# Performance work log

Measured on AMD Instinct MI355X. Metric: run time of the kernel, lower is better.

## Reference

```python
import jax, jax.numpy as jnp
import numpy as np

N = 20000
IN_CH = 2048      # 64 * (768/24)
HID = 512
LAT = 128
KW = 24           # conv1d kernel == stride
COUT = 64
NEG_SLOPE = 0.2
BN_EPS = 1e-5


def gatv2(x, src, dst, Wl, bl, Wr, br, att, bias, n_nodes):
    # GATv2Conv (PyG semantics, 1 head): e_ij = att . leaky_relu(Wl x_j + Wr x_i)
    xl = x @ Wl + bl                      # [N, out] source-side features
    xr = x @ Wr + br                      # [N, out] target-side features
    e = jax.nn.leaky_relu(xl[src] + xr[dst], NEG_SLOPE) @ att   # [E]
    m = jax.ops.segment_max(e, dst, num_segments=n_nodes)       # per-target max
    a = jnp.exp(e - m[dst])
    s = jax.ops.segment_sum(a, dst, num_segments=n_nodes)
    alpha = a / (s[dst] + 1e-16)
    out = jax.ops.segment_sum(xl[src] * alpha[:, None], dst, num_segments=n_nodes)
    return out + bias


def setup_inputs() -> dict:
    key = jax.random.key(0)
    ks = jax.random.split(key, 16)
    x = jax.random.normal(ks[0], (N, 24, 32), dtype=jnp.float32)
    edge_index = jax.random.randint(ks[1], (2, 320000), 0, N, dtype=jnp.int32)
    sc = 0.02
    return {
        "x": x,
        "edge_index": edge_index,
        "conv_w": jax.random.normal(ks[2], (COUT, KW), dtype=jnp.float32) * sc,
        "conv_b": jnp.zeros((COUT,), dtype=jnp.float32),
        "W1l": jax.random.normal(ks[3], (IN_CH, HID), dtype=jnp.float32) * sc,
        "b1l": jnp.zeros((HID,), dtype=jnp.float32),
        "W1r": jax.random.normal(ks[4], (IN_CH, HID), dtype=jnp.float32) * sc,
        "b1r": jnp.zeros((HID,), dtype=jnp.float32),
        "att1": jax.random.normal(ks[5], (HID,), dtype=jnp.float32) * sc,
        "bias1": jnp.zeros((HID,), dtype=jnp.float32),
        "gamma": jnp.ones((HID,), dtype=jnp.float32),
        "beta": jnp.zeros((HID,), dtype=jnp.float32),
        "W2l": jax.random.normal(ks[6], (HID, LAT), dtype=jnp.float32) * sc,
        "b2l": jnp.zeros((LAT,), dtype=jnp.float32),
        "W2r": jax.random.normal(ks[7], (HID, LAT), dtype=jnp.float32) * sc,
        "b2r": jnp.zeros((LAT,), dtype=jnp.float32),
        "att2": jax.random.normal(ks[8], (LAT,), dtype=jnp.float32) * sc,
        "bias2": jnp.zeros((LAT,), dtype=jnp.float32),
    }


def reference(x, edge_index, conv_w, conv_b, W1l, b1l, W1r, b1r, att1, bias1,
              gamma, beta, W2l, b2l, W2r, b2r, att2, bias2):
    n = x.shape[0]
    # x.transpose(1,2).flatten(1): [N,24,32] -> [N,32,24] -> [N,768]
    flat = jnp.transpose(x, (0, 2, 1)).reshape(n, -1)
    # Conv1d(1,64,24,stride=24): kernel==stride => reshape into segments of 24
    segs = flat.reshape(n, -1, KW)                       # [N, 32, 24]
    conv = jnp.einsum("ntk,ok->not", segs, conv_w) + conv_b[None, :, None]  # [N,64,32]
    h = conv.reshape(n, -1)                              # [N, 2048] (channel-major like torch .view)

    # add self-loops (PyG GATv2Conv default add_self_loops=True)
    loops = jnp.arange(n, dtype=edge_index.dtype)
    src = jnp.concatenate([edge_index[0], loops])
    dst = jnp.concatenate([edge_index[1], loops])

    h = gatv2(h, src, dst, W1l, b1l, W1r, b1r, att1, bias1, n)
    h = jax.nn.relu(h)
    # BatchNorm1d in training mode: batch stats over nodes, biased variance
    mean = jnp.mean(h, axis=0)
    var = jnp.mean((h - mean) ** 2, axis=0)
    h = gamma * (h - mean) / jnp.sqrt(var + BN_EPS) + beta

    mu = gatv2(h, src, dst, W2l, b2l, W2r, b2r, att2, bias2, n)
    return mu
```

## Files before the change

### kernel.cpp

```cpp
#include <hip/hip_runtime.h>
#include <cstdint>
#include <cstddef>
#include <type_traits>

static constexpr int NN   = 20000;
static constexpr int MPAD = 20096;
static constexpr int ERAW = 320000;
static constexpr int ETOT = ERAW + NN;

typedef __attribute__((ext_vector_type(8))) short bf16x8;
typedef __attribute__((ext_vector_type(8))) unsigned short u16x8;
typedef __attribute__((ext_vector_type(4))) float f32x4;

__device__ __forceinline__ unsigned short f2bf(float f) {
  union { float f; unsigned u; } v; v.f = f;
  unsigned r = v.u + 0x7fffu + ((v.u >> 16) & 1u);
  return (unsigned short)(r >> 16);
}
__device__ __forceinline__ float bf2f(unsigned short u) {
  union { unsigned u; float f; } v; v.u = ((unsigned)u) << 16;
  return v.f;
}

__device__ __forceinline__ void gload_lds16(const void* g, void* l) {
  __builtin_amdgcn_global_load_lds(
      (const __attribute__((address_space(1))) unsigned int*)g,
      (__attribute__((address_space(3))) unsigned int*)l, 16, 0, 0);
}

__global__ __launch_bounds__(256) void cast_x_kernel(
    const float* __restrict__ x, unsigned short* __restrict__ xb,
    int* __restrict__ degp, float* __restrict__ stats, float* __restrict__ beff1) {
  int i8 = blockIdx.x * 256 + threadIdx.x;
  if (i8 < NN) degp[i8] = 0;
  if (i8 < 1024) { stats[i8] = 0.f; beff1[i8] = 0.f; }
  size_t base = (size_t)i8 * 8;
  int row = i8 / 96;
  u16x8 o;
  if (row < NN) {
    float4 a = *(const float4*)&x[base];
    float4 b = *(const float4*)&x[base + 4];
    o[0] = f2bf(a.x); o[1] = f2bf(a.y); o[2] = f2bf(a.z); o[3] = f2bf(a.w);
    o[4] = f2bf(b.x); o[5] = f2bf(b.y); o[6] = f2bf(b.z); o[7] = f2bf(b.w);
  } else {
#pragma unroll
    for (int j = 0; j < 8; j++) o[j] = 0;
  }
  *(u16x8*)&xb[base] = o;
}

__global__ __launch_bounds__(256) void weff_kernel(
    const float* __restrict__ conv_w, const float* __restrict__ conv_b,
    const float* __restrict__ W1l, const float* __restrict__ b1l,
    const float* __restrict__ W1r, const float* __restrict__ b1r,
    unsigned short* __restrict__ wc1, float* __restrict__ beff1) {
  __shared__ float ws[64 * 24];
  int t = blockIdx.x;
  int tid = threadIdx.x;
  for (int i = tid; i < 64 * 24; i += 256) ws[i] = conv_w[i];
  __syncthreads();
  int c = blockIdx.y * 128 + (tid >> 1);
  int half = tid & 1;
  const float* W; const float* bb; int cl;
  if (c < 512) { W = W1l; bb = b1l; cl = c; } else { W = W1r; bb = b1r; cl = c - 512; }
  float acc[24];
#pragma unroll
  for (int k = 0; k < 24; k++) acc[k] = 0.f;
  float bacc = (t == 0 && half == 0) ? bb[cl] : 0.f;
  for (int o = half * 32; o < half * 32 + 32; o += 4) {
    float Wv[4];
#pragma unroll
    for (int j = 0; j < 4; j++) Wv[j] = W[(size_t)((o + j) * 32 + t) * 512 + cl];
#pragma unroll
    for (int j = 0; j < 4; j++) {
      bacc += conv_b[o + j] * Wv[j];
#pragma unroll
      for (int k = 0; k < 24; k++) acc[k] += ws[(o + j) * 24 + k] * Wv[j];
    }
  }
#pragma unroll
  for (int k = 0; k < 24; k++) acc[k] += __shfl_xor(acc[k], 1);
  bacc += __shfl_xor(bacc, 1);
  if (half == 0) {
#pragma unroll
    for (int k = 0; k < 24; k++) wc1[(size_t)c * 768 + k * 32 + t] = f2bf(acc[k]);
    atomicAdd(&beff1[c], bacc);
  }
}

__global__ __launch_bounds__(256) void w2fold_kernel(
    const float* __restrict__ stats, const float* __restrict__ gamma,
    const float* __restrict__ beta,
    const float* __restrict__ W2l, const float* __restrict__ b2l,
    const float* __restrict__ W2r, const float* __restrict__ b2r,
    unsigned short* __restrict__ wc2, float* __restrict__ beff2) {
  int c = blockIdx.x;
  const float* W; const float* bb; int cl;
  if (c < 128) { W = W2l; bb = b2l; cl = c; } else { W = W2r; bb = b2r; cl = c - 128; }
  int tid = threadIdx.x, lane = tid & 63, wid = tid >> 6;
  float part = 0.f;
#pragma unroll
  for (int j = 0; j < 2; j++) {
    int k = tid * 2 + j;
    float mean = stats[k] * (1.f / NN);
    float var = stats[512 + k] * (1.f / NN) - mean * mean;
    float rstd = rsqrtf(var + 1e-5f);
    float sc = gamma[k] * rstd;
    float sh = beta[k] - sc * mean;
    float wv = W[(size_t)k * 128 + cl];
    wc2[(size_t)c * 512 + k] = f2bf(sc * wv);
    part += sh * wv;
  }
#pragma unroll
  for (int d = 32; d; d >>= 1) part += __shfl_xor(part, d);
  __shared__ float wsum[4];
  if (lane == 0) wsum[wid] = part;
  __syncthreads();
  if (tid == 0) beff2[c] = bb[cl] + wsum[0] + wsum[1] + wsum[2] + wsum[3];
}

template <typename OutT>
__global__ __launch_bounds__(256, 5) void gemm_kernel(
    const unsigned short* __restrict__ A, const unsigned short* __restrict__ B,
    const float* __restrict__ bias0, const float* __restrict__ bias1,
    OutT* __restrict__ C0, OutT* __restrict__ C1,
    int M, int K, int NT, int nsplit, int swz) {
  __shared__ __align__(16) unsigned short As[128 * 64];
  __shared__ __align__(16) unsigned short Bs[128 * 64];
  int bid = blockIdx.x;
  if (swz) bid = (bid & 7) * (gridDim.x >> 3) + (bid >> 3);
  int tm = bid / NT, tn = bid % NT;
  int tid = threadIdx.x, wid = tid >> 6, lane = tid & 63;
  int wr = wid >> 1, wc = wid & 1;
  const unsigned short* gA = A + (size_t)(tm * 128) * K;
  const unsigned short* gB = B + (size_t)(tn * 128) * K;
  int srow = wid * 8 + (lane >> 3);
  int scol = ((lane & 7) ^ (lane >> 3)) * 8;

  f32x4 acc[4][4];
  f32x4 zero = {0.f, 0.f, 0.f, 0.f};
#pragma unroll
  for (int i = 0; i < 4; i++)
#pragma unroll
    for (int j = 0; j < 4; j++) acc[i][j] = zero;

  int KT = K >> 6;
  for (int kt = 0; kt < KT; ++kt) {
    if (kt) __syncthreads();
    {
      const unsigned short* a0 = gA + (size_t)srow * K + kt * 64 + scol;
      const unsigned short* b0 = gB + (size_t)srow * K + kt * 64 + scol;
#pragma unroll
      for (int i = 0; i < 4; i++)
        gload_lds16(a0 + (size_t)i * 32 * K, &As[i * 2048 + wid * 512]);
#pragma unroll
      for (int i = 0; i < 4; i++)
        gload_lds16(b0 + (size_t)i * 32 * K, &Bs[i * 2048 + wid * 512]);
    }
    asm volatile("s_waitcnt vmcnt(0)" ::: "memory");
    __syncthreads();
#pragma unroll
    for (int kk = 0; kk < 2; kk++) {
      int ko = kk * 32 + (lane >> 4) * 8;
      int kosw = ko ^ ((lane & 7) << 3);
      bf16x8 af[4], bfr[4];
#pragma unroll
      for (int mi = 0; mi < 4; mi++)
        af[mi] = *(const bf16x8*)&As[(wr * 64 + mi * 16 + (lane & 15)) * 64 + kosw];
#pragma unroll
      for (int ni = 0; ni < 4; ni++)
        bfr[ni] = *(const bf16x8*)&Bs[(wc * 64 + ni * 16 + (lane & 15)) * 64 + kosw];
#pragma unroll
      for (int mi = 0; mi < 4; mi++)
#pragma unroll
        for (int ni = 0; ni < 4; ni++)
          acc[mi][ni] = __builtin_amdgcn_mfma_f32_16x16x32_bf16(
              af[mi], bfr[ni], acc[mi][ni], 0, 0, 0);
    }
  }

  int ncol_tile = tn * 128;
  OutT* Cd; const float* bs; int col0;
  if (ncol_tile < nsplit) { Cd = C0; bs = bias0; col0 = ncol_tile; }
  else { Cd = C1; bs = bias1; col0 = ncol_tile - nsplit; }
#pragma unroll
  for (int mi = 0; mi < 4; mi++) {
    int rbase = tm * 128 + wr * 64 + mi * 16 + (lane >> 4) * 4;
#pragma unroll
    for (int ni = 0; ni < 4; ni++) {
      int c = col0 + wc * 64 + ni * 16 + (lane & 15);
      float bv = bs[c];
#pragma unroll
      for (int j = 0; j < 4; j++) {
        int r = rbase + j;
        if (r < M) {
          float v = acc[mi][ni][j] + bv;
          if constexpr (sizeof(OutT) == 2) Cd[(size_t)r * nsplit + c] = f2bf(v);
          else Cd[(size_t)r * nsplit + c] = v;
        }
      }
    }
  }
}

__global__ void hist_kernel(const int* __restrict__ dst, int* deg, int E) {
  int e = blockIdx.x * 256 + threadIdx.x;
  if (e < E) atomicAdd(&deg[dst[e]], 1);
}
__global__ __launch_bounds__(1024) void scan1_kernel(
    const int* __restrict__ deg, int* __restrict__ off, int* __restrict__ btot, int n) {
  __shared__ int wsum[16];
  int tid = threadIdx.x, lane = tid & 63, w = tid >> 6;
  int i = blockIdx.x * 1024 + tid;
  int v = (i < n) ? deg[i] + 1 : 0;
  int s = v;
#pragma unroll
  for (int d = 1; d < 64; d <<= 1) {
    int t = __shfl_up(s, d);
    if (lane >= d) s += t;
  }
  if (lane == 63) wsum[w] = s;
  __syncthreads();
  if (w == 0 && lane < 16) {
    int t = wsum[lane];
#pragma unroll
    for (int d = 1; d < 16; d <<= 1) {
      int u = __shfl_up(t, d);
      if (lane >= d) t += u;
    }
    wsum[lane] = t;
  }
  __syncthreads();
  int incl = (w ? wsum[w - 1] : 0) + s;
  if (i < n) off[i] = incl - v;
  if (tid == 1023) btot[blockIdx.x] = incl;
}
__global__ void scan2_kernel(const int* __restrict__ btot, int* __restrict__ gbase,
                             int* __restrict__ off, int nb, int n) {
  int lane = threadIdx.x;
  int v = lane < nb ? btot[lane] : 0;
  int s = v;
#pragma unroll
  for (int d = 1; d < 64; d <<= 1) {
    int t = __shfl_up(s, d);
    if (lane >= d) s += t;
  }
  if (lane < nb) gbase[lane] = s - v;
  if (lane == nb - 1) off[n] = s;
}
__global__ __launch_bounds__(1024) void scan3_kernel(
    int* __restrict__ off, int* __restrict__ cursor,
    const int* __restrict__ gbase, int* __restrict__ esrc, int n) {
  int i = blockIdx.x * 1024 + threadIdx.x;
  if (i < n) {
    int v = off[i] + gbase[blockIdx.x];
    off[i] = v;
    cursor[i] = v + 1;
    esrc[v] = i;
  }
}
__global__ void scatter_kernel(const int* __restrict__ src, const int* __restrict__ dst,
                               int* cursor, int* __restrict__ esrc, int E) {
  int e = blockIdx.x * 256 + threadIdx.x;
  if (e < E) {
    int pos = atomicAdd(&cursor[dst[e]], 1);
    esrc[pos] = src[e];
  }
}

template <int VPL, typename OutT>
__global__ __launch_bounds__(256) void gat_agg_kernel(
    const unsigned short* __restrict__ xl, const unsigned short* __restrict__ xr,
    const float* __restrict__ att, const float* __restrict__ bias,
    const int* __restrict__ off, const int* __restrict__ esrc,
    OutT* __restrict__ out, int n, int do_relu) {
  constexpr int C = VPL * 64;
  using RawT = std::conditional_t<VPL == 8, uint4, unsigned int>;
  int node = blockIdx.x * 4 + (threadIdx.x >> 6);
  int lane = threadIdx.x & 63;
  int base = lane * VPL;
  if (node >= n) {
#pragma unroll
    for (int v = 0; v < VPL; v++) out[(size_t)node * C + base + v] = OutT(0);
    return;
  }
  float xrv[VPL], attv[VPL];
#pragma unroll
  for (int v = 0; v < VPL; v++) {
    xrv[v] = bf2f(xr[(size_t)node * C + base + v]);
    attv[v] = att[base + v];
  }
  auto cvt = [](RawT r, float* xv) {
    if constexpr (VPL == 8) {
      unsigned u[4] = {r.x, r.y, r.z, r.w};
#pragma unroll
      for (int i = 0; i < 4; i++) {
        xv[2 * i]     = __uint_as_float(u[i] << 16);
        xv[2 * i + 1] = __uint_as_float(u[i] & 0xffff0000u);
      }
    } else {
      xv[0] = __uint_as_float(r << 16);
      xv[1] = __uint_as_float(r & 0xffff0000u);
    }
  };
  auto score = [&](const float* xv) {
    float p = 0.f;
#pragma unroll
    for (int v = 0; v < VPL; v++) {
      float t = xv[v] + xrv[v];
      p += attv[v] * fmaxf(t, 0.2f * t);
    }
    return p;
  };
  float s0 = 0.f, s1 = 0.f;
  float acc0[VPL], acc1[VPL];
#pragma unroll
  for (int v = 0; v < VPL; v++) { acc0[v] = 0.f; acc1[v] = 0.f; }
  int e0 = off[node], e1 = off[node + 1];
  int e = e0;
  for (; e + 3 < e1; e += 4) {
    int s0i = esrc[e], s1i = esrc[e + 1], s2i = esrc[e + 2], s3i = esrc[e + 3];
    RawT r0 = *(const RawT*)(xl + (size_t)s0i * C + base);
    RawT r1 = *(const RawT*)(xl + (size_t)s1i * C + base);
    RawT r2 = *(const RawT*)(xl + (size_t)s2i * C + base);
    RawT r3 = *(const RawT*)(xl + (size_t)s3i * C + base);
    float x0[VPL], x1[VPL], x2[VPL], x3[VPL];
    cvt(r0, x0); cvt(r1, x1); cvt(r2, x2); cvt(r3, x3);
    float p0 = score(x0), p1 = score(x1), p2 = score(x2), p3 = score(x3);
    p0 += __shfl_xor(p0, 32); p1 += __shfl_xor(p1, 32);
    p2 += __shfl_xor(p2, 32); p3 += __shfl_xor(p3, 32);
    float a = (lane & 32) ? p1 : p0;
    float b = (lane & 32) ? p3 : p2;
    a += __shfl_xor(a, 16); b += __shfl_xor(b, 16);
    float cpk = (lane & 16) ? b : a;
    cpk += __shfl_xor(cpk, 8); cpk += __shfl_xor(cpk, 4);
    cpk += __shfl_xor(cpk, 2); cpk += __shfl_xor(cpk, 1);
    float w = __expf(cpk);
    float w0 = __shfl(w, 0),  w2 = __shfl(w, 16);
    float w1 = __shfl(w, 32), w3 = __shfl(w, 48);
    s0 += w0 + w2; s1 += w1 + w3;
#pragma unroll
    for (int v = 0; v < VPL; v++) {
      acc0[v] += w0 * x0[v] + w2 * x2[v];
      acc1[v] += w1 * x1[v] + w3 * x3[v];
    }
  }
  for (; e < e1; ++e) {
    RawT r0 = *(const RawT*)(xl + (size_t)esrc[e] * C + base);
    float x0[VPL];
    cvt(r0, x0);
    float p0 = score(x0);
#pragma unroll
    for (int d2 = 32; d2; d2 >>= 1) p0 += __shfl_xor(p0, d2);
    float w0 = __expf(p0);
    s0 += w0;
#pragma unroll
    for (int v = 0; v < VPL; v++) acc0[v] += w0 * x0[v];
  }
  float inv = 1.f / (s0 + s1 + 1e-16f);
#pragma unroll
  for (int v = 0; v < VPL; v++) {
    float o = (acc0[v] + acc1[v]) * inv + bias[base + v];
    if (do_relu) o = fmaxf(o, 0.f);
    if constexpr (sizeof(OutT) == 2) out[(size_t)node * C + base + v] = f2bf(o);
    else out[(size_t)node * C + base + v] = o;
  }
}

__global__ __launch_bounds__(256) void bn_stats_kernel(
    const unsigned short* __restrict__ h1, float* __restrict__ stats, int n) {
  int tid = threadIdx.x;
  int c0 = tid * 2;
  int r0 = blockIdx.x * 64;
  int r1 = r0 + 64 < n ? r0 + 64 : n;
  float s0 = 0, q0 = 0, s1 = 0, q1 = 0;
  for (int r = r0; r < r1; ++r) {
    unsigned u = *(const unsigned*)&h1[(size_t)r * 512 + c0];
    float a = __uint_as_float(u << 16);
    float b = __uint_as_float(u & 0xffff0000u);
    s0 += a; q0 += a * a; s1 += b; q1 += b * b;
  }
  atomicAdd(&stats[c0], s0);
  atomicAdd(&stats[c0 + 1], s1);
  atomicAdd(&stats[512 + c0], q0);
  atomicAdd(&stats[512 + c0 + 1], q1);
}

extern "C" void kernel_launch(void* const* d_in, const int* in_sizes, int n_in,
                              void* d_out, int out_size, void* d_ws, size_t ws_size,
                              hipStream_t stream) {
  (void)in_sizes; (void)n_in; (void)out_size; (void)ws_size;
  const float* x      = (const float*)d_in[0];
  const int*   ei     = (const int*)d_in[1];
  const float* conv_w = (const float*)d_in[2];
  const float* conv_b = (const float*)d_in[3];
  const float* W1l    = (const float*)d_in[4];
  const float* b1l    = (const float*)d_in[5];
  const float* W1r    = (const float*)d_in[6];
  const float* b1r    = (const float*)d_in[7];
  const float* att1   = (const float*)d_in[8];
  const float* bias1  = (const float*)d_in[9];
  const float* gamma  = (const float*)d_in[10];
  const float* beta   = (const float*)d_in[11];
  const float* W2l    = (const float*)d_in[12];
  const float* b2l    = (const float*)d_in[13];
  const float* W2r    = (const float*)d_in[14];
  const float* b2r    = (const float*)d_in[15];
  const float* att2   = (const float*)d_in[16];
  const float* bias2  = (const float*)d_in[17];

  char* ws = (char*)d_ws;
  size_t off = 0;
  auto alloc = [&](size_t bytes) {
    size_t r = off;
    off += (bytes + 255) & ~(size_t)255;
    return r;
  };
  size_t o_xb   = alloc((size_t)MPAD * 768 * 2);
  size_t o_wc1  = alloc((size_t)1024 * 768 * 2);
  size_t o_wc2  = alloc((size_t)256 * 512 * 2);
  size_t o_xl1  = alloc((size_t)NN * 512 * 2);
  size_t o_xr1  = alloc((size_t)NN * 512 * 2);
  size_t o_h1   = alloc((size_t)MPAD * 512 * 2);
  size_t o_xl2  = alloc((size_t)NN * 128 * 2);
  size_t o_xr2  = alloc((size_t)NN * 128 * 2);
  size_t o_off  = alloc((size_t)(NN + 1) * 4);
  size_t o_cur  = alloc((size_t)NN * 4);
  size_t o_deg  = alloc((size_t)NN * 4);
  size_t o_esrc = alloc((size_t)ETOT * 4);
  size_t o_stats = alloc((size_t)1024 * 4);
  size_t o_beff1 = alloc((size_t)1024 * 4);
  size_t o_beff2 = alloc((size_t)256 * 4);
  size_t o_btot  = alloc((size_t)64 * 4);
  size_t o_gbase = alloc((size_t)64 * 4);

  unsigned short* xb  = (unsigned short*)(ws + o_xb);
  unsigned short* wc1 = (unsigned short*)(ws + o_wc1);
  unsigned short* wc2 = (unsigned short*)(ws + o_wc2);
  unsigned short* xl1 = (unsigned short*)(ws + o_xl1);
  unsigned short* xr1 = (unsigned short*)(ws + o_xr1);
  unsigned short* h1  = (unsigned short*)(ws + o_h1);
  unsigned short* xl2 = (unsigned short*)(ws + o_xl2);
  unsigned short* xr2 = (unsigned short*)(ws + o_xr2);
  int* offp  = (int*)(ws + o_off);
  int* curp  = (int*)(ws + o_cur);
  int* degp  = (int*)(ws + o_deg);
  int* esrc  = (int*)(ws + o_esrc);
  float* stats = (float*)(ws + o_stats);
  float* beff1 = (float*)(ws + o_beff1);
  float* beff2 = (float*)(ws + o_beff2);
  int* btot  = (int*)(ws + o_btot);
  int* gbase = (int*)(ws + o_gbase);

  const int* src_raw = ei;
  const int* dst_raw = ei + ERAW;
  float* mu = (float*)d_out;

  cast_x_kernel<<<(MPAD * 96) / 256, 256, 0, stream>>>(x, xb, degp, stats, beff1);
  weff_kernel<<<dim3(32, 8), 256, 0, stream>>>(conv_w, conv_b, W1l, b1l, W1r, b1r, wc1, beff1);

  hist_kernel<<<(ERAW + 255) / 256, 256, 0, stream>>>(dst_raw, degp, ERAW);
  const int NB = (NN + 1023) / 1024;
  scan1_kernel<<<NB, 1024, 0, stream>>>(degp, offp, btot, NN);
  scan2_kernel<<<1, 64, 0, stream>>>(btot, gbase, offp, NB, NN);
  scan3_kernel<<<NB, 1024, 0, stream>>>(offp, curp, gbase, esrc, NN);
  scatter_kernel<<<(ERAW + 255) / 256, 256, 0, stream>>>(src_raw, dst_raw, curp, esrc, ERAW);

  gemm_kernel<unsigned short><<<(MPAD / 128) * (1024 / 128), 256, 0, stream>>>(
      xb, wc1, beff1, beff1 + 512, xl1, xr1, NN, 768, 8, 512, 1);
  gat_agg_kernel<8, unsigned short><<<MPAD / 4, 256, 0, stream>>>(
      xl1, xr1, att1, bias1, offp, esrc, h1, NN, 1);

  bn_stats_kernel<<<(NN + 63) / 64, 256, 0, stream>>>(h1, stats, NN);
  w2fold_kernel<<<256, 256, 0, stream>>>(stats, gamma, beta, W2l, b2l, W2r, b2r, wc2, beff2);

  gemm_kernel<unsigned short><<<(MPAD / 128) * (256 / 128), 256, 0, stream>>>(
      h1, wc2, beff2, beff2 + 128, xl2, xr2, NN, 512, 2, 128, 0);
  gat_agg_kernel<2, float><<<NN / 4, 256, 0, stream>>>(
      xl2, xr2, att2, bias2, offp, esrc, mu, NN, 0);
}
```

Baseline: 266.7 us.

## Fuse histogram into weff, merge scans with last-block sync, batch edge index loads

The degree histogram moves into the weight-fold kernel, and the three scan kernels become one kernel that uses a last-block-done counter and a spin-wait flag to publish block offsets. Together these remove several tiny launches. The GAT aggregation kernels now read 64 edge indices per wave in one coalesced load and broadcast them with shuffles, and they launch 1024-thread blocks holding 16 nodes each. The spin-wait assumes all 20 scan blocks are resident at the same time, which holds here but is fragile, and the larger blocks may change occupancy.

```diff
diff --git a/kernel.cpp b/kernel.cpp
--- a/kernel.cpp
+++ b/kernel.cpp
@@ -30,10 +30,12 @@
 
 __global__ __launch_bounds__(256) void cast_x_kernel(
     const float* __restrict__ x, unsigned short* __restrict__ xb,
-    int* __restrict__ degp, float* __restrict__ stats, float* __restrict__ beff1) {
+    int* __restrict__ degp, float* __restrict__ stats, float* __restrict__ beff1,
+    int* __restrict__ syncp) {
   int i8 = blockIdx.x * 256 + threadIdx.x;
   if (i8 < NN) degp[i8] = 0;
   if (i8 < 1024) { stats[i8] = 0.f; beff1[i8] = 0.f; }
+  if (i8 < 2) syncp[i8] = 0;
   size_t base = (size_t)i8 * 8;
   int row = i8 / 96;
   u16x8 o;
@@ -53,7 +55,11 @@
     const float* __restrict__ conv_w, const float* __restrict__ conv_b,
     const float* __restrict__ W1l, const float* __restrict__ b1l,
     const float* __restrict__ W1r, const float* __restrict__ b1r,
-    unsigned short* __restrict__ wc1, float* __restrict__ beff1) {
+    unsigned short* __restrict__ wc1, float* __restrict__ beff1,
+    const int* __restrict__ dst, int* __restrict__ deg, int E) {
+  int gid = (blockIdx.y * 32 + blockIdx.x) * 256 + threadIdx.x;
+  for (int e = gid; e < E; e += 65536) atomicAdd(&deg[dst[e]], 1);
+
   __shared__ float ws[64 * 24];
   int t = blockIdx.x;
   int tid = threadIdx.x;
@@ -203,13 +209,12 @@
   }
 }
 
-__global__ void hist_kernel(const int* __restrict__ dst, int* deg, int E) {
-  int e = blockIdx.x * 256 + threadIdx.x;
-  if (e < E) atomicAdd(&deg[dst[e]], 1);
-}
-__global__ __launch_bounds__(1024) void scan1_kernel(
-    const int* __restrict__ deg, int* __restrict__ off, int* __restrict__ btot, int n) {
+__global__ __launch_bounds__(1024) void scan_kernel(
+    const int* __restrict__ deg, int* __restrict__ off, int* __restrict__ cursor,
+    int* __restrict__ esrc, int* __restrict__ btot, int* __restrict__ syncp,
+    int n, int nb) {
   __shared__ int wsum[16];
+  __shared__ int amLast;
   int tid = threadIdx.x, lane = tid & 63, w = tid >> 6;
   int i = blockIdx.x * 1024 + tid;
   int v = (i < n) ? deg[i] + 1 : 0;
@@ -232,31 +237,37 @@
   }
   __syncthreads();
   int incl = (w ? wsum[w - 1] : 0) + s;
-  if (i < n) off[i] = incl - v;
-  if (tid == 1023) btot[blockIdx.x] = incl;
-}
-__global__ void scan2_kernel(const int* __restrict__ btot, int* __restrict__ gbase,
-                             int* __restrict__ off, int nb, int n) {
-  int lane = threadIdx.x;
-  int v = lane < nb ? btot[lane] : 0;
-  int s = v;
-#pragma unroll
-  for (int d = 1; d < 64; d <<= 1) {
-    int t = __shfl_up(s, d);
-    if (lane >= d) s += t;
-  }
-  if (lane < nb) gbase[lane] = s - v;
-  if (lane == nb - 1) off[n] = s;
-}
-__global__ __launch_bounds__(1024) void scan3_kernel(
-    int* __restrict__ off, int* __restrict__ cursor,
-    const int* __restrict__ gbase, int* __restrict__ esrc, int n) {
-  int i = blockIdx.x * 1024 + threadIdx.x;
+  if (tid == 0) btot[blockIdx.x] = wsum[15];
+  __threadfence();
+  if (tid == 0) amLast = (atomicAdd(&syncp[0], 1) == nb - 1);
+  __syncthreads();
+  if (amLast) {
+    __threadfence();
+    if (w == 0) {
+      int bv = (lane < nb) ? atomicAdd(&btot[lane], 0) : 0;
+      int bs = bv;
+#pragma unroll
+      for (int d = 1; d < 64; d <<= 1) {
+        int u = __shfl_up(bs, d);
+        if (lane >= d) bs += u;
+      }
+      if (lane < nb) btot[lane] = bs - bv;
+      if (lane == nb - 1) off[n] = bs;
+    }
+    __syncthreads();
+    __threadfence();
+    if (tid == 0) atomicExch(&syncp[1], 1);
+  }
+  if (tid == 0) {
+    while (atomicAdd(&syncp[1], 0) == 0) { }
+  }
+  __syncthreads();
+  int gb = atomicAdd(&btot[blockIdx.x], 0);
   if (i < n) {
-    int v = off[i] + gbase[blockIdx.x];
-    off[i] = v;
-    cursor[i] = v + 1;
-    esrc[v] = i;
+    int val = incl - v + gb;
+    off[i] = val;
+    cursor[i] = val + 1;
+    esrc[val] = i;
   }
 }
 __global__ void scatter_kernel(const int* __restrict__ src, const int* __restrict__ dst,
@@ -269,14 +280,14 @@
 }
 
 template <int VPL, typename OutT>
-__global__ __launch_bounds__(256) void gat_agg_kernel(
+__global__ __launch_bounds__(1024) void gat_agg_kernel(
     const unsigned short* __restrict__ xl, const unsigned short* __restrict__ xr,
     const float* __restrict__ att, const float* __restrict__ bias,
     const int* __restrict__ off, const int* __restrict__ esrc,
     OutT* __restrict__ out, int n, int do_relu) {
   constexpr int C = VPL * 64;
   using RawT = std::conditional_t<VPL == 8, uint4, unsigned int>;
-  int node = blockIdx.x * 4 + (threadIdx.x >> 6);
+  int node = blockIdx.x * 16 + (threadIdx.x >> 6);
   int lane = threadIdx.x & 63;
   int base = lane * VPL;
   if (node >= n) {
@@ -317,45 +328,51 @@
 #pragma unroll
   for (int v = 0; v < VPL; v++) { acc0[v] = 0.f; acc1[v] = 0.f; }
   int e0 = off[node], e1 = off[node + 1];
-  int e = e0;
-  for (; e + 3 < e1; e += 4) {
-    int s0i = esrc[e], s1i = esrc[e + 1], s2i = esrc[e + 2], s3i = esrc[e + 3];
-    RawT r0 = *(const RawT*)(xl + (size_t)s0i * C + base);
-    RawT r1 = *(const RawT*)(xl + (size_t)s1i * C + base);
-    RawT r2 = *(const RawT*)(xl + (size_t)s2i * C + base);
-    RawT r3 = *(const RawT*)(xl + (size_t)s3i * C + base);
-    float x0[VPL], x1[VPL], x2[VPL], x3[VPL];
-    cvt(r0, x0); cvt(r1, x1); cvt(r2, x2); cvt(r3, x3);
-    float p0 = score(x0), p1 = score(x1), p2 = score(x2), p3 = score(x3);
-    p0 += __shfl_xor(p0, 32); p1 += __shfl_xor(p1, 32);
-    p2 += __shfl_xor(p2, 32); p3 += __shfl_xor(p3, 32);
-    float a = (lane & 32) ? p1 : p0;
-    float b = (lane & 32) ? p3 : p2;
-    a += __shfl_xor(a, 16); b += __shfl_xor(b, 16);
-    float cpk = (lane & 16) ? b : a;
-    cpk += __shfl_xor(cpk, 8); cpk += __shfl_xor(cpk, 4);
-    cpk += __shfl_xor(cpk, 2); cpk += __shfl_xor(cpk, 1);
-    float w = __expf(cpk);
-    float w0 = __shfl(w, 0),  w2 = __shfl(w, 16);
-    float w1 = __shfl(w, 32), w3 = __shfl(w, 48);
-    s0 += w0 + w2; s1 += w1 + w3;
-#pragma unroll
-    for (int v = 0; v < VPL; v++) {
-      acc0[v] += w0 * x0[v] + w2 * x2[v];
-      acc1[v] += w1 * x1[v] + w3 * x3[v];
-    }
-  }
-  for (; e < e1; ++e) {
-    RawT r0 = *(const RawT*)(xl + (size_t)esrc[e] * C + base);
-    float x0[VPL];
-    cvt(r0, x0);
-    float p0 = score(x0);
-#pragma unroll
-    for (int d2 = 32; d2; d2 >>= 1) p0 += __shfl_xor(p0, d2);
-    float w0 = __expf(p0);
-    s0 += w0;
-#pragma unroll
-    for (int v = 0; v < VPL; v++) acc0[v] += w0 * x0[v];
+  for (int cb = e0; cb < e1; cb += 64) {
+    int cnt = (e1 - cb) < 64 ? (e1 - cb) : 64;
+    int myidx = (cb + lane < e1) ? esrc[cb + lane] : 0;
+    int j = 0;
+    for (; j + 3 < cnt; j += 4) {
+      int s0i = __shfl(myidx, j),     s1i = __shfl(myidx, j + 1);
+      int s2i = __shfl(myidx, j + 2), s3i = __shfl(myidx, j + 3);
+      RawT r0 = *(const RawT*)(xl + (size_t)s0i * C + base);
+      RawT r1 = *(const RawT*)(xl + (size_t)s1i * C + base);
+      RawT r2 = *(const RawT*)(xl + (size_t)s2i * C + base);
+      RawT r3 = *(const RawT*)(xl + (size_t)s3i * C + base);
+      float x0[VPL], x1[VPL], x2[VPL], x3[VPL];
+      cvt(r0, x0); cvt(r1, x1); cvt(r2, x2); cvt(r3, x3);
+      float p0 = score(x0), p1 = score(x1), p2 = score(x2), p3 = score(x3);
+      p0 += __shfl_xor(p0, 32); p1 += __shfl_xor(p1, 32);
+      p2 += __shfl_xor(p2, 32); p3 += __shfl_xor(p3, 32);
+      float a = (lane & 32) ? p1 : p0;
+      float b = (lane & 32) ? p3 : p2;
+      a += __shfl_xor(a, 16); b += __shfl_xor(b, 16);
+      float cpk = (lane & 16) ? b : a;
+      cpk += __shfl_xor(cpk, 8); cpk += __shfl_xor(cpk, 4);
+      cpk += __shfl_xor(cpk, 2); cpk += __shfl_xor(cpk, 1);
+      float w = __expf(cpk);
+      float w0 = __shfl(w, 0),  w2 = __shfl(w, 16);
+      float w1 = __shfl(w, 32), w3 = __shfl(w, 48);
+      s0 += w0 + w2; s1 += w1 + w3;
+#pragma unroll
+      for (int v = 0; v < VPL; v++) {
+        acc0[v] += w0 * x0[v] + w2 * x2[v];
+        acc1[v] += w1 * x1[v] + w3 * x3[v];
+      }
+    }
+    for (; j < cnt; ++j) {
+      int sj = __shfl(myidx, j);
+      RawT r0 = *(const RawT*)(xl + (size_t)sj * C + base);
+      float x0[VPL];
+      cvt(r0, x0);
+      float p0 = score(x0);
+#pragma unroll
+      for (int d2 = 32; d2; d2 >>= 1) p0 += __shfl_xor(p0, d2);
+      float w0 = __expf(p0);
+      s0 += w0;
+#pragma unroll
+      for (int v = 0; v < VPL; v++) acc0[v] += w0 * x0[v];
+    }
   }
   float inv = 1.f / (s0 + s1 + 1e-16f);
 #pragma unroll
@@ -432,7 +449,7 @@
   size_t o_beff1 = alloc((size_t)1024 * 4);
   size_t o_beff2 = alloc((size_t)256 * 4);
   size_t o_btot  = alloc((size_t)64 * 4);
-  size_t o_gbase = alloc((size_t)64 * 4);
+  size_t o_sync  = alloc((size_t)16 * 4);
 
   unsigned short* xb  = (unsigned short*)(ws + o_xb);
   unsigned short* wc1 = (unsigned short*)(ws + o_wc1);
@@ -450,25 +467,23 @@
   float* beff1 = (float*)(ws + o_beff1);
   float* beff2 = (float*)(ws + o_beff2);
   int* btot  = (int*)(ws + o_btot);
-  int* gbase = (int*)(ws + o_gbase);
+  int* syncp = (int*)(ws + o_sync);
 
   const int* src_raw = ei;
   const int* dst_raw = ei + ERAW;
   float* mu = (float*)d_out;
 
-  cast_x_kernel<<<(MPAD * 96) / 256, 256, 0, stream>>>(x, xb, degp, stats, beff1);
-  weff_kernel<<<dim3(32, 8), 256, 0, stream>>>(conv_w, conv_b, W1l, b1l, W1r, b1r, wc1, beff1);
-
-  hist_kernel<<<(ERAW + 255) / 256, 256, 0, stream>>>(dst_raw, degp, ERAW);
+  cast_x_kernel<<<(MPAD * 96) / 256, 256, 0, stream>>>(x, xb, degp, stats, beff1, syncp);
+  weff_kernel<<<dim3(32, 8), 256, 0, stream>>>(conv_w, conv_b, W1l, b1l, W1r, b1r,
+                                               wc1, beff1, dst_raw, degp, ERAW);
+
   const int NB = (NN + 1023) / 1024;
-  scan1_kernel<<<NB, 1024, 0, stream>>>(degp, offp, btot, NN);
-  scan2_kernel<<<1, 64, 0, stream>>>(btot, gbase, offp, NB, NN);
-  scan3_kernel<<<NB, 1024, 0, stream>>>(offp, curp, gbase, esrc, NN);
+  scan_kernel<<<NB, 1024, 0, stream>>>(degp, offp, curp, esrc, btot, syncp, NN, NB);
   scatter_kernel<<<(ERAW + 255) / 256, 256, 0, stream>>>(src_raw, dst_raw, curp, esrc, ERAW);
 
   gemm_kernel<unsigned short><<<(MPAD / 128) * (1024 / 128), 256, 0, stream>>>(
       xb, wc1, beff1, beff1 + 512, xl1, xr1, NN, 768, 8, 512, 1);
-  gat_agg_kernel<8, unsigned short><<<MPAD / 4, 256, 0, stream>>>(
+  gat_agg_kernel<8, unsigned short><<<MPAD / 16, 1024, 0, stream>>>(
       xl1, xr1, att1, bias1, offp, esrc, h1, NN, 1);
 
   bn_stats_kernel<<<(NN + 63) / 64, 256, 0, stream>>>(h1, stats, NN);
@@ -476,6 +491,6 @@
 
   gemm_kernel<unsigned short><<<(MPAD / 128) * (256 / 128), 256, 0, stream>>>(
       h1, wc2, beff2, beff2 + 128, xl2, xr2, NN, 512, 2, 128, 0);
-  gat_agg_kernel<2, float><<<NN / 4, 256, 0, stream>>>(
+  gat_agg_kernel<2, float><<<NN / 16, 1024, 0, stream>>>(
       xl2, xr2, att2, bias2, offp, esrc, mu, NN, 0);
 }
```

Measured after the change: 281.8 us. 5.6% more time.

## Split each node's edge list across two wavefronts with LDS reduction

Applied to the files above, without the earlier changes.

The GAT aggregation kernel now assigns two wavefronts per destination node, each handling alternating edges (stride 2), and combines partial accumulators and softmax sums through shared memory before one wave writes the output. Grid size doubles to keep two nodes per 256-thread block. The aim is more memory-level parallelism on the irregular gathers, with shorter per-wave loops and better latency hiding. The cost is an extra LDS round trip and __syncthreads per block, plus one of the two waves sitting idle during the epilogue.

```diff
diff --git a/kernel.cpp b/kernel.cpp
--- a/kernel.cpp
+++ b/kernel.cpp
@@ -276,18 +276,17 @@
     OutT* __restrict__ out, int n, int do_relu) {
   constexpr int C = VPL * 64;
   using RawT = std::conditional_t<VPL == 8, uint4, unsigned int>;
-  int node = blockIdx.x * 4 + (threadIdx.x >> 6);
-  int lane = threadIdx.x & 63;
+  int tid = threadIdx.x;
+  int nslot = tid >> 7;
+  int w = (tid >> 6) & 1;
+  int lane = tid & 63;
+  int node = blockIdx.x * 2 + nslot;
   int base = lane * VPL;
-  if (node >= n) {
-#pragma unroll
-    for (int v = 0; v < VPL; v++) out[(size_t)node * C + base + v] = OutT(0);
-    return;
-  }
+  bool real = node < n;
   float xrv[VPL], attv[VPL];
 #pragma unroll
   for (int v = 0; v < VPL; v++) {
-    xrv[v] = bf2f(xr[(size_t)node * C + base + v]);
+    xrv[v] = real ? bf2f(xr[(size_t)node * C + base + v]) : 0.f;
     attv[v] = att[base + v];
   }
   auto cvt = [](RawT r, float* xv) {
@@ -316,10 +315,11 @@
   float acc0[VPL], acc1[VPL];
 #pragma unroll
   for (int v = 0; v < VPL; v++) { acc0[v] = 0.f; acc1[v] = 0.f; }
-  int e0 = off[node], e1 = off[node + 1];
-  int e = e0;
-  for (; e + 3 < e1; e += 4) {
-    int s0i = esrc[e], s1i = esrc[e + 1], s2i = esrc[e + 2], s3i = esrc[e + 3];
+  int e0 = 0, e1 = 0;
+  if (real) { e0 = off[node]; e1 = off[node + 1]; }
+  int e = e0 + w;
+  for (; e + 6 < e1; e += 8) {
+    int s0i = esrc[e], s1i = esrc[e + 2], s2i = esrc[e + 4], s3i = esrc[e + 6];
     RawT r0 = *(const RawT*)(xl + (size_t)s0i * C + base);
     RawT r1 = *(const RawT*)(xl + (size_t)s1i * C + base);
     RawT r2 = *(const RawT*)(xl + (size_t)s2i * C + base);
@@ -335,9 +335,9 @@
     float cpk = (lane & 16) ? b : a;
     cpk += __shfl_xor(cpk, 8); cpk += __shfl_xor(cpk, 4);
     cpk += __shfl_xor(cpk, 2); cpk += __shfl_xor(cpk, 1);
-    float w = __expf(cpk);
-    float w0 = __shfl(w, 0),  w2 = __shfl(w, 16);
-    float w1 = __shfl(w, 32), w3 = __shfl(w, 48);
+    float wv = __expf(cpk);
+    float w0 = __shfl(wv, 0),  w2 = __shfl(wv, 16);
+    float w1 = __shfl(wv, 32), w3 = __shfl(wv, 48);
     s0 += w0 + w2; s1 += w1 + w3;
 #pragma unroll
     for (int v = 0; v < VPL; v++) {
@@ -345,7 +345,7 @@
       acc1[v] += w1 * x1[v] + w3 * x3[v];
     }
   }
-  for (; e < e1; ++e) {
+  for (; e < e1; e += 2) {
     RawT r0 = *(const RawT*)(xl + (size_t)esrc[e] * C + base);
     float x0[VPL];
     cvt(r0, x0);
@@ -357,13 +357,26 @@
 #pragma unroll
     for (int v = 0; v < VPL; v++) acc0[v] += w0 * x0[v];
   }
-  float inv = 1.f / (s0 + s1 + 1e-16f);
-#pragma unroll
-  for (int v = 0; v < VPL; v++) {
-    float o = (acc0[v] + acc1[v]) * inv + bias[base + v];
-    if (do_relu) o = fmaxf(o, 0.f);
-    if constexpr (sizeof(OutT) == 2) out[(size_t)node * C + base + v] = f2bf(o);
-    else out[(size_t)node * C + base + v] = o;
+  __shared__ float part[2][2][64 * (VPL + 1)];
+  float* mine = &part[nslot][w][lane * (VPL + 1)];
+#pragma unroll
+  for (int v = 0; v < VPL; v++) mine[v] = acc0[v] + acc1[v];
+  mine[VPL] = s0 + s1;
+  __syncthreads();
+  if (w == 0) {
+    const float* oth = &part[nslot][1][lane * (VPL + 1)];
+    float stot = mine[VPL] + oth[VPL];
+    float inv = 1.f / (stot + 1e-16f);
+#pragma unroll
+    for (int v = 0; v < VPL; v++) {
+      float o = 0.f;
+      if (real) {
+        o = (mine[v] + oth[v]) * inv + bias[base + v];
+        if (do_relu) o = fmaxf(o, 0.f);
+      }
+      if constexpr (sizeof(OutT) == 2) out[(size_t)node * C + base + v] = f2bf(o);
+      else out[(size_t)node * C + base + v] = o;
+    }
   }
 }
 
@@ -468,7 +481,7 @@
 
   gemm_kernel<unsigned short><<<(MPAD / 128) * (1024 / 128), 256, 0, stream>>>(
       xb, wc1, beff1, beff1 + 512, xl1, xr1, NN, 768, 8, 512, 1);
-  gat_agg_kernel<8, unsigned short><<<MPAD / 4, 256, 0, stream>>>(
+  gat_agg_kernel<8, unsigned short><<<MPAD / 2, 256, 0, stream>>>(
       xl1, xr1, att1, bias1, offp, esrc, h1, NN, 1);
 
   bn_stats_kernel<<<(NN + 63) / 64, 256, 0, stream>>>(h1, stats, NN);
@@ -476,6 +489,6 @@
 
   gemm_kernel<unsigned short><<<(MPAD / 128) * (256 / 128), 256, 0, stream>>>(
       h1, wc2, beff2, beff2 + 128, xl2, xr2, NN, 512, 2, 128, 0);
-  gat_agg_kernel<2, float><<<NN / 4, 256, 0, stream>>>(
+  gat_agg_kernel<2, float><<<NN / 2, 256, 0, stream>>>(
       xl2, xr2, att2, bias2, offp, esrc, mu, NN, 0);
 }
```

After: 315.2 us. +18.2%, slower.
